# Optimization experiments

Measured on AMD Instinct MI355X. Metric: run time of the kernel, lower is better.

The kernel has to match this reference:

```python
import jax, jax.numpy as jnp
import numpy as np

K = 6                      # max_displacement / pad_size
WIN = 2 * K + 1            # displacement window side
D = WIN * WIN              # number of affinity channels (169)


def setup_inputs() -> dict:
    key = jax.random.key(0)
    k1, k2 = jax.random.split(key)
    aff = jax.random.normal(k1, (4, D, 192, 192), dtype=jnp.float32)
    input2 = jax.random.normal(k2, (4, 64, 192, 192), dtype=jnp.float32)
    return {"aff": aff, "input2": input2}


def reference(aff, input2):
    # output[b,c,y,x] = sum_{dy,dx in [-k,k]} aff[b, idx(dy,dx), y, x]
    #                   * input2_zeropad[b, c, y+dy, x+dx]
    # Scanned over the (2k+1)^2 displacements to avoid materializing the
    # [B, D, C, H, W] cost-volume intermediate.
    B, C, H, W = input2.shape
    Dn = aff.shape[1]
    win = int(round(Dn ** 0.5))
    k = (win - 1) // 2
    padded = jnp.pad(input2, ((0, 0), (0, 0), (k, k), (k, k)))  # [B,C,H+2k,W+2k]
    aff_t = jnp.transpose(aff, (1, 0, 2, 3))  # [D,B,H,W]
    ds = jnp.arange(Dn)

    def body(acc, xs):
        d, a = xs                      # a: [B,H,W]
        dy = d // win                  # 0..2k (offset into padded rows)
        dx = d % win                   # 0..2k (offset into padded cols)
        patch = jax.lax.dynamic_slice(padded, (0, 0, dy, dx), (B, C, H, W))
        return acc + a[:, None, :, :] * patch, None

    out, _ = jax.lax.scan(body, jnp.zeros_like(input2), (ds, aff_t))
    return out
```

## Files before the change

### kernel.cpp

```cpp
#include <hip/hip_runtime.h>


#define KD   6
#define WIN  13
#define ND   169
#define NB   4
#define NC   64
#define NH   192
#define NW   192
#define XH   64
#define PITCHW 42
#define BUFW (NC * PITCHW)
#define NTH  256

typedef _Float16 half2v __attribute__((ext_vector_type(2)));

static __device__ __forceinline__ half2v h2(unsigned u) {
    return __builtin_bit_cast(half2v, u);
}
static __device__ __forceinline__ unsigned pk(float a, float b) {
    return __builtin_bit_cast(unsigned, __builtin_amdgcn_cvt_pkrtz(a, b));
}

#if __has_builtin(__builtin_amdgcn_fdot2)
#define FDOT2(a, b, c) __builtin_amdgcn_fdot2((a), (b), (c), false)
#else
static __device__ __forceinline__ float fdot2_fb(half2v a, half2v b, float c) {
    return fmaf((float)a.x, (float)b.x, fmaf((float)a.y, (float)b.y, c));
}
#define FDOT2(a, b, c) fdot2_fb((a), (b), (c))
#endif

static __device__ __forceinline__ void aff_issue(const float* __restrict__ ap,
                                                 float4 (&Af)[13]) {
#pragma unroll
    for (int dx = 0; dx < WIN; ++dx)
        Af[dx] = *(const float4*)&ap[(size_t)dx * (NH * NW)];
}

static __device__ __forceinline__ void aff_pack(const float4 (&Af)[13],
                                                unsigned (&P)[7][4]) {
#pragma unroll
    for (int m = 0; m < 6; ++m) {
        P[m][0] = pk(Af[2*m].x, Af[2*m+1].x);
        P[m][1] = pk(Af[2*m].y, Af[2*m+1].y);
        P[m][2] = pk(Af[2*m].z, Af[2*m+1].z);
        P[m][3] = pk(Af[2*m].w, Af[2*m+1].w);
    }
    P[6][0] = pk(Af[12].x, 0.f);
    P[6][1] = pk(Af[12].y, 0.f);
    P[6][2] = pk(Af[12].z, 0.f);
    P[6][3] = pk(Af[12].w, 0.f);
}

static __device__ __forceinline__ void pass_y(const unsigned* __restrict__ wpb,
                                              const unsigned (&P)[7][4],
                                              float (&acc)[4][4]) {
#pragma unroll
    for (int i = 0; i < 4; ++i) {
        const unsigned* wp = wpb + i * (16 * PITCHW);
        const uint2 t0 = *(const uint2*)&wp[0];
        const uint2 t1 = *(const uint2*)&wp[2];
        const uint2 t2 = *(const uint2*)&wp[4];
        const uint2 t3 = *(const uint2*)&wp[6];
        const uint2 t4 = *(const uint2*)&wp[8];
        const unsigned P1 = t0.y, P2 = t1.x, P3 = t1.y, P4 = t2.x;
        const unsigned P5 = t2.y, P6 = t3.x, P7 = t3.y, P8 = t4.x;
        const unsigned P9 = t4.y;
        const unsigned S1 = (P1 >> 16) | (P2 << 16);
        const unsigned S2 = (P2 >> 16) | (P3 << 16);
        const unsigned S3 = (P3 >> 16) | (P4 << 16);
        const unsigned S4 = (P4 >> 16) | (P5 << 16);
        const unsigned S5 = (P5 >> 16) | (P6 << 16);
        const unsigned S6 = (P6 >> 16) | (P7 << 16);
        const unsigned S7 = (P7 >> 16) | (P8 << 16);
        const unsigned S8 = (P8 >> 16) | (P9 << 16);

        float a0 = acc[i][0], a1 = acc[i][1], a2 = acc[i][2], a3 = acc[i][3];
        a0 = FDOT2(h2(P[0][0]), h2(P1), a0);
        a0 = FDOT2(h2(P[1][0]), h2(P2), a0);
        a0 = FDOT2(h2(P[2][0]), h2(P3), a0);
        a0 = FDOT2(h2(P[3][0]), h2(P4), a0);
        a0 = FDOT2(h2(P[4][0]), h2(P5), a0);
        a0 = FDOT2(h2(P[5][0]), h2(P6), a0);
        a0 = FDOT2(h2(P[6][0]), h2(P7), a0);
        a1 = FDOT2(h2(P[0][1]), h2(S1), a1);
        a1 = FDOT2(h2(P[1][1]), h2(S2), a1);
        a1 = FDOT2(h2(P[2][1]), h2(S3), a1);
        a1 = FDOT2(h2(P[3][1]), h2(S4), a1);
        a1 = FDOT2(h2(P[4][1]), h2(S5), a1);
        a1 = FDOT2(h2(P[5][1]), h2(S6), a1);
        a1 = FDOT2(h2(P[6][1]), h2(S7), a1);
        a2 = FDOT2(h2(P[0][2]), h2(P2), a2);
        a2 = FDOT2(h2(P[1][2]), h2(P3), a2);
        a2 = FDOT2(h2(P[2][2]), h2(P4), a2);
        a2 = FDOT2(h2(P[3][2]), h2(P5), a2);
        a2 = FDOT2(h2(P[4][2]), h2(P6), a2);
        a2 = FDOT2(h2(P[5][2]), h2(P7), a2);
        a2 = FDOT2(h2(P[6][2]), h2(P8), a2);
        a3 = FDOT2(h2(P[0][3]), h2(S2), a3);
        a3 = FDOT2(h2(P[1][3]), h2(S3), a3);
        a3 = FDOT2(h2(P[2][3]), h2(S4), a3);
        a3 = FDOT2(h2(P[3][3]), h2(S5), a3);
        a3 = FDOT2(h2(P[4][3]), h2(S6), a3);
        a3 = FDOT2(h2(P[5][3]), h2(S7), a3);
        a3 = FDOT2(h2(P[6][3]), h2(S8), a3);
        acc[i][0] = a0; acc[i][1] = a1; acc[i][2] = a2; acc[i][3] = a3;
    }
}

__global__ __launch_bounds__(NTH, 2)
void mxassemble(const float* __restrict__ aff,
                const float* __restrict__ in2,
                float* __restrict__ out) {
    __shared__ unsigned ldsw[2 * BUFW];

    const int bx = blockIdx.x;
    const int g  = bx & 7;
    const int k  = bx >> 3;
    const int b  = k / 12;
    const int by = 12 * g + (k - 12 * b);
    const int y0 = 2 * by;
    const int xb = blockIdx.y;
    const int X0 = xb * XH;

    const int t    = threadIdx.x;
    const int l    = t & 63;
    const int wv   = t >> 6;
    const int cg   = l & 15;
    const int xs   = l >> 4;
    const int slot = wv * 4 + xs;
    const int x0   = X0 + slot * 4;

    if (xb != 1) {
        const int w0 = (xb == 0) ? 0 : 36;
        if (t < NC * 2) {
            const int c = t >> 1, qq = t & 1;
            *(uint2*)&ldsw[c * PITCHW + w0 + 2 * qq]        = make_uint2(0u, 0u);
            *(uint2*)&ldsw[BUFW + c * PITCHW + w0 + 2 * qq] = make_uint2(0u, 0u);
        }
    }

    int wadr[5], goff[5];
#pragma unroll
    for (int s = 0; s < 5; ++s) {
        const int ii = t + NTH * s;
        const int c  = ii / 20;
        const int q  = ii - 20 * c;
        const int xg = X0 - 8 + 4 * q;
        const bool ok = (xg >= 0) && (xg < NW);
        wadr[s] = ok ? (c * PITCHW + 2 * q) : -1;
        goff[s] = c * (NH * NW) + xg;
    }

    float acc0[4][4], acc1[4][4];
#pragma unroll
    for (int i = 0; i < 4; ++i)
#pragma unroll
        for (int j = 0; j < 4; ++j) { acc0[i][j] = 0.f; acc1[i][j] = 0.f; }

    const float* in2_b  = in2 + (size_t)b * NC * NH * NW;
    const float* aff_y0 = aff + (size_t)b * ND * NH * NW + (size_t)y0 * NW + x0;
    const float* aff_y1 = aff_y0 + NW;
    const int wbase = cg * PITCHW + 2 * slot;

    float4 Af[13];
    unsigned PA[7][4], PB[7][4];

    aff_issue(aff_y0, Af);
    if (y0 - KD >= 0) {
        const float* p = in2_b + (size_t)(y0 - KD) * NW;
        float4 Sv[5];
#pragma unroll
        for (int s = 0; s < 5; ++s)
            if (wadr[s] >= 0) Sv[s] = *(const float4*)&p[goff[s]];
#pragma unroll
        for (int s = 0; s < 5; ++s)
            if (wadr[s] >= 0) {
                uint2 w; w.x = pk(Sv[s].x, Sv[s].y); w.y = pk(Sv[s].z, Sv[s].w);
                *(uint2*)&ldsw[wadr[s]] = w;
            }
    }
    aff_pack(Af, PA);
    __syncthreads();

    const float* apB = aff_y1;
    const float* apA = aff_y0 + (size_t)(WIN * NH * NW);

    for (int rr = 0; rr < 14; ++rr) {
        const int r = y0 - KD + rr;
        const bool rowvalid = (r >= 0) && (r < NH);
        const int rn = r + 1;
        const bool stage_next = (rr < 13) && (rn >= 0) && (rn < NH);
        unsigned* curw = ldsw + ((rr & 1) ? BUFW : 0);
        unsigned* nxtw = ldsw + ((rr & 1) ? 0 : BUFW);

        if (rr < 13) aff_issue(apB, Af);
        float4 Sv[5];
        if (stage_next) {
            const float* p = in2_b + (size_t)rn * NW;
#pragma unroll
            for (int s = 0; s < 5; ++s)
                if (wadr[s] >= 0) Sv[s] = *(const float4*)&p[goff[s]];
        }
        if (rowvalid && rr >= 1) pass_y(curw + wbase, PB, acc1);
        if (rr < 13) aff_pack(Af, PB);
        if (stage_next) {
#pragma unroll
            for (int s = 0; s < 5; ++s)
                if (wadr[s] >= 0) {
                    uint2 w; w.x = pk(Sv[s].x, Sv[s].y); w.y = pk(Sv[s].z, Sv[s].w);
                    *(uint2*)&nxtw[wadr[s]] = w;
                }
        }
        if (rr < 12) aff_issue(apA, Af);
        if (rowvalid && rr <= 12) pass_y(curw + wbase, PA, acc0);
        if (rr < 12) aff_pack(Af, PA);

        apB += (size_t)(WIN * NH * NW);
        apA += (size_t)(WIN * NH * NW);
        __syncthreads();
    }

    float* ob = out + (((size_t)b * NC + cg) * NH + y0) * NW + x0;
#pragma unroll
    for (int i = 0; i < 4; ++i) {
        *(float4*)&ob[(size_t)(16 * i) * NH * NW] =
            make_float4(acc0[i][0], acc0[i][1], acc0[i][2], acc0[i][3]);
        *(float4*)&ob[(size_t)(16 * i) * NH * NW + NW] =
            make_float4(acc1[i][0], acc1[i][1], acc1[i][2], acc1[i][3]);
    }
}

extern "C" void kernel_launch(void* const* d_in, const int* in_sizes, int n_in,
                              void* d_out, int out_size, void* d_ws, size_t ws_size,
                              hipStream_t stream) {
    const float* aff = (const float*)d_in[0];
    const float* in2 = (const float*)d_in[1];
    float* outp = (float*)d_out;
    dim3 grid(384, 3, 1);
    dim3 block(NTH);
    hipLaunchKernelGGL(mxassemble, grid, block, 0, stream, aff, in2, outp);
}
```

Before: 309.2 us.

## Switch to one output row per block with fp32 FMA on affinities

Replaces the two-row-per-block fp16 dot2 scheme with a single output row per block. The affinity values now stay in fp32 and are FMA'd against staged fp16 input values converted back to float. The grid is flattened to cover every row, with an occupancy hint of 3-4 waves per EU. This cuts register pressure and aff packing, but doubles staging of input2 rows per output row and uses scalar FMAs instead of packed dot2, roughly doubling arithmetic instructions.

After: 404.9 us. 30.9% more time.

```diff
diff --git a/kernel.cpp b/kernel.cpp
--- a/kernel.cpp
+++ b/kernel.cpp
@@ -21,108 +21,27 @@
 static __device__ __forceinline__ unsigned pk(float a, float b) {
     return __builtin_bit_cast(unsigned, __builtin_amdgcn_cvt_pkrtz(a, b));
 }
-
-#if __has_builtin(__builtin_amdgcn_fdot2)
-#define FDOT2(a, b, c) __builtin_amdgcn_fdot2((a), (b), (c), false)
-#else
-static __device__ __forceinline__ float fdot2_fb(half2v a, half2v b, float c) {
-    return fmaf((float)a.x, (float)b.x, fmaf((float)a.y, (float)b.y, c));
-}
-#define FDOT2(a, b, c) fdot2_fb((a), (b), (c))
-#endif
-
-static __device__ __forceinline__ void aff_issue(const float* __restrict__ ap,
-                                                 float4 (&Af)[13]) {
-#pragma unroll
-    for (int dx = 0; dx < WIN; ++dx)
-        Af[dx] = *(const float4*)&ap[(size_t)dx * (NH * NW)];
+static __device__ __forceinline__ float hget(unsigned w, int sel) {
+    const half2v h = h2(w);
+    return sel ? (float)h.y : (float)h.x;
 }
 
-static __device__ __forceinline__ void aff_pack(const float4 (&Af)[13],
-                                                unsigned (&P)[7][4]) {
-#pragma unroll
-    for (int m = 0; m < 6; ++m) {
-        P[m][0] = pk(Af[2*m].x, Af[2*m+1].x);
-        P[m][1] = pk(Af[2*m].y, Af[2*m+1].y);
-        P[m][2] = pk(Af[2*m].z, Af[2*m+1].z);
-        P[m][3] = pk(Af[2*m].w, Af[2*m+1].w);
-    }
-    P[6][0] = pk(Af[12].x, 0.f);
-    P[6][1] = pk(Af[12].y, 0.f);
-    P[6][2] = pk(Af[12].z, 0.f);
-    P[6][3] = pk(Af[12].w, 0.f);
-}
-
-static __device__ __forceinline__ void pass_y(const unsigned* __restrict__ wpb,
-                                              const unsigned (&P)[7][4],
-                                              float (&acc)[4][4]) {
-#pragma unroll
-    for (int i = 0; i < 4; ++i) {
-        const unsigned* wp = wpb + i * (16 * PITCHW);
-        const uint2 t0 = *(const uint2*)&wp[0];
-        const uint2 t1 = *(const uint2*)&wp[2];
-        const uint2 t2 = *(const uint2*)&wp[4];
-        const uint2 t3 = *(const uint2*)&wp[6];
-        const uint2 t4 = *(const uint2*)&wp[8];
-        const unsigned P1 = t0.y, P2 = t1.x, P3 = t1.y, P4 = t2.x;
-        const unsigned P5 = t2.y, P6 = t3.x, P7 = t3.y, P8 = t4.x;
-        const unsigned P9 = t4.y;
-        const unsigned S1 = (P1 >> 16) | (P2 << 16);
-        const unsigned S2 = (P2 >> 16) | (P3 << 16);
-        const unsigned S3 = (P3 >> 16) | (P4 << 16);
-        const unsigned S4 = (P4 >> 16) | (P5 << 16);
-        const unsigned S5 = (P5 >> 16) | (P6 << 16);
-        const unsigned S6 = (P6 >> 16) | (P7 << 16);
-        const unsigned S7 = (P7 >> 16) | (P8 << 16);
-        const unsigned S8 = (P8 >> 16) | (P9 << 16);
-
-        float a0 = acc[i][0], a1 = acc[i][1], a2 = acc[i][2], a3 = acc[i][3];
-        a0 = FDOT2(h2(P[0][0]), h2(P1), a0);
-        a0 = FDOT2(h2(P[1][0]), h2(P2), a0);
-        a0 = FDOT2(h2(P[2][0]), h2(P3), a0);
-        a0 = FDOT2(h2(P[3][0]), h2(P4), a0);
-        a0 = FDOT2(h2(P[4][0]), h2(P5), a0);
-        a0 = FDOT2(h2(P[5][0]), h2(P6), a0);
-        a0 = FDOT2(h2(P[6][0]), h2(P7), a0);
-        a1 = FDOT2(h2(P[0][1]), h2(S1), a1);
-        a1 = FDOT2(h2(P[1][1]), h2(S2), a1);
-        a1 = FDOT2(h2(P[2][1]), h2(S3), a1);
-        a1 = FDOT2(h2(P[3][1]), h2(S4), a1);
-        a1 = FDOT2(h2(P[4][1]), h2(S5), a1);
-        a1 = FDOT2(h2(P[5][1]), h2(S6), a1);
-        a1 = FDOT2(h2(P[6][1]), h2(S7), a1);
-        a2 = FDOT2(h2(P[0][2]), h2(P2), a2);
-        a2 = FDOT2(h2(P[1][2]), h2(P3), a2);
-        a2 = FDOT2(h2(P[2][2]), h2(P4), a2);
-        a2 = FDOT2(h2(P[3][2]), h2(P5), a2);
-        a2 = FDOT2(h2(P[4][2]), h2(P6), a2);
-        a2 = FDOT2(h2(P[5][2]), h2(P7), a2);
-        a2 = FDOT2(h2(P[6][2]), h2(P8), a2);
-        a3 = FDOT2(h2(P[0][3]), h2(S2), a3);
-        a3 = FDOT2(h2(P[1][3]), h2(S3), a3);
-        a3 = FDOT2(h2(P[2][3]), h2(S4), a3);
-        a3 = FDOT2(h2(P[3][3]), h2(S5), a3);
-        a3 = FDOT2(h2(P[4][3]), h2(S6), a3);
-        a3 = FDOT2(h2(P[5][3]), h2(S7), a3);
-        a3 = FDOT2(h2(P[6][3]), h2(S8), a3);
-        acc[i][0] = a0; acc[i][1] = a1; acc[i][2] = a2; acc[i][3] = a3;
-    }
-}
-
-__global__ __launch_bounds__(NTH, 2)
+__global__ __launch_bounds__(NTH)
+__attribute__((amdgpu_waves_per_eu(3, 4)))
 void mxassemble(const float* __restrict__ aff,
                 const float* __restrict__ in2,
                 float* __restrict__ out) {
     __shared__ unsigned ldsw[2 * BUFW];
 
-    const int bx = blockIdx.x;
-    const int g  = bx & 7;
-    const int k  = bx >> 3;
-    const int b  = k / 12;
-    const int by = 12 * g + (k - 12 * b);
-    const int y0 = 2 * by;
-    const int xb = blockIdx.y;
-    const int X0 = xb * XH;
+    const int bx  = blockIdx.x;
+    const int g   = bx & 7;
+    const int m   = bx >> 3;
+    const int b   = m / 72;
+    const int r72 = m - 72 * b;
+    const int xb  = r72 / 24;
+    const int yl  = r72 - 24 * xb;
+    const int y   = 24 * g + yl;
+    const int X0  = xb * XH;
 
     const int t    = threadIdx.x;
     const int l    = t & 63;
@@ -153,82 +72,100 @@
         goff[s] = c * (NH * NW) + xg;
     }
 
-    float acc0[4][4], acc1[4][4];
+    float acc[4][4];
 #pragma unroll
     for (int i = 0; i < 4; ++i)
 #pragma unroll
-        for (int j = 0; j < 4; ++j) { acc0[i][j] = 0.f; acc1[i][j] = 0.f; }
+        for (int j = 0; j < 4; ++j) acc[i][j] = 0.f;
 
-    const float* in2_b  = in2 + (size_t)b * NC * NH * NW;
-    const float* aff_y0 = aff + (size_t)b * ND * NH * NW + (size_t)y0 * NW + x0;
-    const float* aff_y1 = aff_y0 + NW;
+    const float* in2_b = in2 + (size_t)b * NC * NH * NW;
+    const float* apc   = aff + (size_t)b * ND * NH * NW + (size_t)y * NW + x0;
     const int wbase = cg * PITCHW + 2 * slot;
 
-    float4 Af[13];
-    unsigned PA[7][4], PB[7][4];
-
-    aff_issue(aff_y0, Af);
-    if (y0 - KD >= 0) {
-        const float* p = in2_b + (size_t)(y0 - KD) * NW;
-        float4 Sv[5];
+    {
+        const int r0 = y - KD;
+        if (r0 >= 0) {
+            const float* p = in2_b + (size_t)r0 * NW;
+            float4 Sv[5];
 #pragma unroll
-        for (int s = 0; s < 5; ++s)
-            if (wadr[s] >= 0) Sv[s] = *(const float4*)&p[goff[s]];
+            for (int s = 0; s < 5; ++s)
+                if (wadr[s] >= 0) Sv[s] = *(const float4*)&p[goff[s]];
 #pragma unroll
-        for (int s = 0; s < 5; ++s)
-            if (wadr[s] >= 0) {
-                uint2 w; w.x = pk(Sv[s].x, Sv[s].y); w.y = pk(Sv[s].z, Sv[s].w);
-                *(uint2*)&ldsw[wadr[s]] = w;
-            }
+            for (int s = 0; s < 5; ++s)
+                if (wadr[s] >= 0) {
+                    uint2 w; w.x = pk(Sv[s].x, Sv[s].y); w.y = pk(Sv[s].z, Sv[s].w);
+                    *(uint2*)&ldsw[wadr[s]] = w;
+                }
+        }
     }
-    aff_pack(Af, PA);
     __syncthreads();
 
-    const float* apB = aff_y1;
-    const float* apA = aff_y0 + (size_t)(WIN * NH * NW);
+    for (int rr = 0; rr < WIN; ++rr) {
+        const unsigned* cur = ldsw + ((rr & 1) ? BUFW : 0);
+        unsigned*       nxt = ldsw + ((rr & 1) ? 0 : BUFW);
+        const int  r  = y - KD + rr;
+        const bool pv = (r >= 0) && (r < NH);
+        const int  rn = r + 1;
+        const bool sv = (rr < WIN - 1) && (rn >= 0) && (rn < NH);
 
-    for (int rr = 0; rr < 14; ++rr) {
-        const int r = y0 - KD + rr;
-        const bool rowvalid = (r >= 0) && (r < NH);
-        const int rn = r + 1;
-        const bool stage_next = (rr < 13) && (rn >= 0) && (rn < NH);
-        unsigned* curw = ldsw + ((rr & 1) ? BUFW : 0);
-        unsigned* nxtw = ldsw + ((rr & 1) ? 0 : BUFW);
-
-        if (rr < 13) aff_issue(apB, Af);
+        alignas(16) float Afr[WIN][4];
+        if (pv) {
+#pragma unroll
+            for (int dx = 0; dx < WIN; ++dx)
+                *(float4*)&Afr[dx][0] =
+                    *(const float4*)&apc[(size_t)dx * (NH * NW)];
+        }
         float4 Sv[5];
-        if (stage_next) {
+        if (sv) {
             const float* p = in2_b + (size_t)rn * NW;
 #pragma unroll
             for (int s = 0; s < 5; ++s)
                 if (wadr[s] >= 0) Sv[s] = *(const float4*)&p[goff[s]];
         }
-        if (rowvalid && rr >= 1) pass_y(curw + wbase, PB, acc1);
-        if (rr < 13) aff_pack(Af, PB);
-        if (stage_next) {
+        __builtin_amdgcn_sched_barrier(0);
+
+        if (pv) {
+            const unsigned* wb = cur + wbase;
+#pragma unroll
+            for (int i = 0; i < 4; ++i) {
+                const unsigned* wp = wb + i * (16 * PITCHW);
+                unsigned W[10];
+                *(uint2*)&W[0] = *(const uint2*)&wp[0];
+                *(uint2*)&W[2] = *(const uint2*)&wp[2];
+                *(uint2*)&W[4] = *(const uint2*)&wp[4];
+                *(uint2*)&W[6] = *(const uint2*)&wp[6];
+                *(uint2*)&W[8] = *(const uint2*)&wp[8];
+#pragma unroll
+                for (int j = 0; j < 4; ++j) {
+                    float a = acc[i][j];
+#pragma unroll
+                    for (int dx = 0; dx < WIN; ++dx) {
+                        const int mm = j + dx + 2;
+                        a = fmaf(Afr[dx][j], hget(W[mm >> 1], mm & 1), a);
+                    }
+                    acc[i][j] = a;
+                }
+            }
+        }
+
+        if (sv) {
 #pragma unroll
             for (int s = 0; s < 5; ++s)
                 if (wadr[s] >= 0) {
                     uint2 w; w.x = pk(Sv[s].x, Sv[s].y); w.y = pk(Sv[s].z, Sv[s].w);
-                    *(uint2*)&nxtw[wadr[s]] = w;
+                    *(uint2*)&nxt[wadr[s]] = w;
                 }
         }
-        if (rr < 12) aff_issue(apA, Af);
-        if (rowvalid && rr <= 12) pass_y(curw + wbase, PA, acc0);
-        if (rr < 12) aff_pack(Af, PA);
 
-        apB += (size_t)(WIN * NH * NW);
-        apA += (size_t)(WIN * NH * NW);
+        apc += (size_t)WIN * NH * NW;
         __syncthreads();
     }
 
-    float* ob = out + (((size_t)b * NC + cg) * NH + y0) * NW + x0;
+    float* ob = out + (((size_t)b * NC + cg) * NH + y) * NW + x0;
 #pragma unroll
     for (int i = 0; i < 4; ++i) {
         *(float4*)&ob[(size_t)(16 * i) * NH * NW] =
-            make_float4(acc0[i][0], acc0[i][1], acc0[i][2], acc0[i][3]);
-        *(float4*)&ob[(size_t)(16 * i) * NH * NW + NW] =
-            make_float4(acc1[i][0], acc1[i][1], acc1[i][2], acc1[i][3]);
+            make_float4(acc[i][0], acc[i][1], acc[i][2], acc[i][3]);
     }
 }
 
@@ -238,7 +175,7 @@
     const float* aff = (const float*)d_in[0];
     const float* in2 = (const float*)d_in[1];
     float* outp = (float*)d_out;
-    dim3 grid(384, 3, 1);
+    dim3 grid(NB * NH * 3, 1, 1);
     dim3 block(NTH);
     hipLaunchKernelGGL(mxassemble, grid, block, 0, stream, aff, in2, outp);
 }
```
